# Kernel optimization log

Hardware: AMD Instinct MI355X
Metric: run time of the kernel (lower is better)

## Reference

```python
import jax, jax.numpy as jnp
import numpy as np
import math

B, S, D = 4, 2048, 1024
N_HEADS = 16
D_FF = 4096
T_DIM = 256
KEEP_RATIO = 0.7
EPS = 1e-5


def _layernorm(x):
    mu = jnp.mean(x, axis=-1, keepdims=True)
    var = jnp.mean((x - mu) ** 2, axis=-1, keepdims=True)
    return (x - mu) * jax.lax.rsqrt(var + EPS)


def _ada_ln(x, cond, W, b):
    # cond: (B, T_DIM); W: (2D, T_DIM)
    p = jax.nn.silu(cond) @ W.T + b            # (B, 2D)
    gamma, beta = jnp.split(p, 2, axis=-1)
    return _layernorm(x) * (1.0 + gamma[:, None, :]) + beta[:, None, :]


def _mha(h, in_w, in_b, out_w, out_b):
    b, s, d = h.shape
    hd = d // N_HEADS
    qkv = h @ in_w.T + in_b                     # (b, s, 3d)
    q, k, v = jnp.split(qkv, 3, axis=-1)
    def heads(t):
        return t.reshape(b, s, N_HEADS, hd).transpose(0, 2, 1, 3)
    q, k, v = heads(q), heads(k), heads(v)
    scores = jnp.einsum('bhqd,bhkd->bhqk', q, k) / math.sqrt(hd)
    attn = jax.nn.softmax(scores, axis=-1)
    o = jnp.einsum('bhqk,bhkd->bhqd', attn, v)  # (b, h, s, hd)
    o = o.transpose(0, 2, 1, 3).reshape(b, s, d)
    return o @ out_w.T + out_b


def setup_inputs() -> dict:
    key = jax.random.key(0)
    ks = jax.random.split(key, 24)
    sc = 0.02
    return {
        'x': jax.random.normal(ks[0], (B, S, D), jnp.float32),
        't_emb': jax.random.normal(ks[1], (B, T_DIM), jnp.float32),
        'tr_w1': jax.random.normal(ks[2], (32, D), jnp.float32) * sc,
        'tr_b1': jnp.zeros((32,), jnp.float32),
        'tr_w2': jax.random.normal(ks[3], (1, 32), jnp.float32) * sc,
        'tr_b2': jnp.zeros((1,), jnp.float32),
        'ln1_w': jax.random.normal(ks[4], (2 * D, T_DIM), jnp.float32) * sc,
        'ln1_b': jnp.zeros((2 * D,), jnp.float32),
        'ln2_w': jax.random.normal(ks[5], (2 * D, T_DIM), jnp.float32) * sc,
        'ln2_b': jnp.zeros((2 * D,), jnp.float32),
        'in_proj_w': jax.random.normal(ks[6], (3 * D, D), jnp.float32) * sc,
        'in_proj_b': jnp.zeros((3 * D,), jnp.float32),
        'out_w': jax.random.normal(ks[7], (D, D), jnp.float32) * sc,
        'out_b': jnp.zeros((D,), jnp.float32),
        'ffn_w1': jax.random.normal(ks[8], (D_FF, D), jnp.float32) * sc,
        'ffn_b1': jnp.zeros((D_FF,), jnp.float32),
        'ffn_w2': jax.random.normal(ks[9], (D, D_FF), jnp.float32) * sc,
        'ffn_b2': jnp.zeros((D,), jnp.float32),
        # torch inits gates to zero; use small randn so the block is non-trivial
        'gate_attn': jax.random.normal(ks[10], (1, 1, D), jnp.float32) * sc,
        'gate_ffn': jax.random.normal(ks[11], (1, 1, D), jnp.float32) * sc,
    }


def reference(x, t_emb, tr_w1, tr_b1, tr_w2, tr_b2, ln1_w, ln1_b, ln2_w, ln2_b,
              in_proj_w, in_proj_b, out_w, out_b, ffn_w1, ffn_b1, ffn_w2, ffn_b2,
              gate_attn, gate_ffn):
    b, s, d = x.shape
    num_keep = max(int(s * KEEP_RATIO), 1)

    # token importance on detached x (stop_gradient mirrors x.detach())
    xd = jax.lax.stop_gradient(x)
    imp = jax.nn.silu(xd @ tr_w1.T + tr_b1) @ tr_w2.T + tr_b2  # (b, s, 1)
    imp = imp[..., 0]
    _, idx = jax.lax.top_k(imp, num_keep)
    idx = jnp.sort(idx, axis=-1)                               # (b, num_keep)

    x_sel = jnp.take_along_axis(x, idx[..., None], axis=1)     # (b, k, d)

    h = _ada_ln(x_sel, t_emb, ln1_w, ln1_b)
    h = _mha(h, in_proj_w, in_proj_b, out_w, out_b)
    x_sel = x_sel + gate_attn * h

    h = _ada_ln(x_sel, t_emb, ln2_w, ln2_b)
    h = jax.nn.gelu(h @ ffn_w1.T + ffn_b1, approximate=False) @ ffn_w2.T + ffn_b2
    x_sel = x_sel + gate_ffn * h

    batch_idx = jnp.arange(b)[:, None]
    return x.at[batch_idx, idx].set(x_sel)
```

## Files before the change

### kernel.cpp

```cpp
#include <hip/hip_runtime.h>
#include <hip/hip_bf16.h>
#include <cmath>
#include <cstdint>

typedef __bf16 bf16;
typedef __bf16 bf16x8 __attribute__((ext_vector_type(8)));
typedef __bf16 bf16x4 __attribute__((ext_vector_type(4)));
typedef float  f32x4  __attribute__((ext_vector_type(4)));

constexpr int B_   = 4;
constexpr int S_   = 2048;
constexpr int D_   = 1024;
constexpr int H_   = 16;
constexpr int DFF_ = 4096;
constexpr int TD_  = 256;
constexpr int KEEP = 1433;
constexpr int M_TOT = B_ * KEEP;
constexpr int MPAD  = 5888;
constexpr int QT64  = (KEEP + 63) / 64;
constexpr int NKV   = (KEEP + 63) / 64;
constexpr float EPS = 1e-5f;
constexpr float QSCALE = 0.18033688011112042f;

__device__ __forceinline__ f32x4 mfma16(bf16x8 a, bf16x8 b, f32x4 c) {
  return __builtin_amdgcn_mfma_f32_16x16x32_bf16(a, b, c, 0, 0, 0);
}

#define GLOAD_LDS(gp, lp)                                                     \
  __builtin_amdgcn_global_load_lds(                                           \
      (const __attribute__((address_space(1))) void*)(gp),                    \
      (__attribute__((address_space(3))) void*)(lp), 16, 0, 0)

__global__ __launch_bounds__(256) void k_prep(
    const float* __restrict__ x, const float* __restrict__ tr_w1,
    double* __restrict__ hidden,
    const float* __restrict__ in_w, const float* __restrict__ out_w,
    const float* __restrict__ f1_w, const float* __restrict__ f2_w,
    bf16* __restrict__ w_in, bf16* __restrict__ w_out,
    bf16* __restrict__ w_f1, bf16* __restrict__ w_f2,
    float* __restrict__ dout,
    const float* __restrict__ temb,
    const float* __restrict__ ln1_w, const float* __restrict__ ln1_b,
    float* __restrict__ p1,
    const float* __restrict__ ln2_w, const float* __restrict__ ln2_b,
    float* __restrict__ p2)
{
  __shared__ double sred[4][64][17];
  const int bid = blockIdx.x;
  if (bid < 2048) {
    const int lane = threadIdx.x & 63, w = threadIdx.x >> 6;
    const int tok0 = (bid & 511) * 16 + w * 4;
    const int u0 = (bid >> 9) * 8;
    const float* xb = x + (size_t)tok0 * D_ + lane * 4;
    const float* wb = tr_w1 + (size_t)u0 * D_ + lane * 4;
    double acc[4][8] = {};
#pragma unroll 2
    for (int c = 0; c < D_; c += 256) {
      float4 xv[4], wv[8];
#pragma unroll
      for (int i = 0; i < 4; ++i)
        xv[i] = *(const float4*)(xb + (size_t)i * D_ + c);
#pragma unroll
      for (int u = 0; u < 8; ++u)
        wv[u] = *(const float4*)(wb + (size_t)u * D_ + c);
#pragma unroll
      for (int i = 0; i < 4; ++i)
#pragma unroll
        for (int u = 0; u < 8; ++u) {
          acc[i][u] += (double)xv[i].x * (double)wv[u].x;
          acc[i][u] += (double)xv[i].y * (double)wv[u].y;
          acc[i][u] += (double)xv[i].z * (double)wv[u].z;
          acc[i][u] += (double)xv[i].w * (double)wv[u].w;
        }
    }
    double* my = &sred[w][0][0];
#pragma unroll
    for (int bt = 0; bt < 2; ++bt) {
#pragma unroll
      for (int a = 0; a < 16; ++a)
        my[lane * 17 + a] = acc[2 * bt + (a >> 3)][a & 7];
      asm volatile("s_waitcnt lgkmcnt(0)" ::: "memory");
      __builtin_amdgcn_sched_barrier(0);
      const int a = lane >> 2, sl = lane & 3;
      const double* rp = my + (sl * 16) * 17 + a;
      double s0 = rp[0]        + rp[17];
      double s1 = rp[2  * 17]  + rp[3  * 17];
      double s2 = rp[4  * 17]  + rp[5  * 17];
      double s3 = rp[6  * 17]  + rp[7  * 17];
      s0 += rp[8  * 17]; s1 += rp[9  * 17];
      s2 += rp[10 * 17]; s3 += rp[11 * 17];
      s0 += rp[12 * 17]; s1 += rp[13 * 17];
      s2 += rp[14 * 17]; s3 += rp[15 * 17];
      double s = (s0 + s1) + (s2 + s3);
      s += __shfl_xor(s, 1);
      s += __shfl_xor(s, 2);
      if (sl == 0)
        hidden[(size_t)(tok0 + 2 * bt + (a >> 3)) * 32 + u0 + (a & 7)] = s;
      asm volatile("s_waitcnt lgkmcnt(0)" ::: "memory");
      __builtin_amdgcn_sched_barrier(0);
    }
  } else if (bid < 3584) {
    const int base = (bid - 2048) * 2048 + threadIdx.x;
#pragma unroll
    for (int k2 = 0; k2 < 8; ++k2) {
      const int g = base + k2 * 256;
      const float* src; bf16* dst; int off;
      if (g < 786432)       { src = in_w;  dst = w_in;  off = g; }
      else if (g < 1048576) { src = out_w; dst = w_out; off = g - 786432; }
      else if (g < 2097152) { src = f1_w;  dst = w_f1;  off = g - 1048576; }
      else                  { src = f2_w;  dst = w_f2;  off = g - 2097152; }
      float4 v = ((const float4*)src)[off];
      bf16x4 o = {(bf16)v.x, (bf16)v.y, (bf16)v.z, (bf16)v.w};
      ((bf16x4*)dst)[off] = o;
    }
  } else if (bid < 4608) {
    const int base = (bid - 3584) * 2048 + threadIdx.x;
    float4 v[8];
#pragma unroll
    for (int k2 = 0; k2 < 8; ++k2) v[k2] = ((const float4*)x)[base + k2 * 256];
#pragma unroll
    for (int k2 = 0; k2 < 8; ++k2) ((float4*)dout)[base + k2 * 256] = v[k2];
  } else {
    int gw = (int)(((bid - 4608) * 256 + threadIdx.x) >> 6);
    const int lane = threadIdx.x & 63;
    const float* W = ln1_w; const float* bias = ln1_b; float* p = p1;
    if (gw >= 8192) { gw -= 8192; W = ln2_w; bias = ln2_b; p = p2; }
    const int b = gw >> 11;
    const int row = gw & 2047;
    const float* te = temb + (size_t)b * TD_;
    const float* wr = W + (size_t)row * TD_;
    float acc = 0.f;
    for (int i = lane; i < TD_; i += 64) {
      float c = te[i];
      acc += (c / (1.f + __expf(-c))) * wr[i];
    }
    for (int o = 32; o > 0; o >>= 1) acc += __shfl_down(acc, o);
    if (lane == 0) p[(size_t)b * 2 * D_ + row] = acc + bias[row];
  }
}

__global__ __launch_bounds__(256) void k_imptail(
    const double* __restrict__ hidden, const float* __restrict__ b1,
    const float* __restrict__ w2, const float* __restrict__ b2,
    double* __restrict__ imp)
{
  const int tok = blockIdx.x * 256 + threadIdx.x;
  const double* hp = hidden + (size_t)tok * 32;
  double r = 0.0;
#pragma unroll
  for (int u = 0; u < 32; ++u) {
    double s = hp[u] + (double)b1[u];
    double sv = s / (1.0 + exp(-s));
    r += sv * (double)w2[u];
  }
  imp[tok] = r + (double)b2[0];
}

__global__ __launch_bounds__(256) void k_rank(const double* __restrict__ imp,
                                              int* __restrict__ rank)
{
  const int b = blockIdx.x >> 5;
  const int seg = blockIdx.x & 31;
  __shared__ double vals[S_];
  const double* ib = imp + (size_t)b * S_;
  for (int i = threadIdx.x; i < S_ / 2; i += 256)
    ((double2*)vals)[i] = ((const double2*)ib)[i];
  __syncthreads();
  const int tl = threadIdx.x >> 2;
  const int part = threadIdx.x & 3;
  const int s = seg * 64 + tl;
  const double v = vals[s];
  int cnt = 0;
  for (int j = part * 512; j < (part + 1) * 512; ++j) {
    double u = vals[j];
    cnt += (u > v) || (u == v && j < s);
  }
  cnt += __shfl_xor(cnt, 1);
  cnt += __shfl_xor(cnt, 2);
  if (part == 0) rank[b * S_ + s] = cnt;
}

__global__ __launch_bounds__(256) void k_compact(const int* __restrict__ rank,
                                                 int* __restrict__ idx)
{
  const int b = blockIdx.x;
  __shared__ int wcnt[4];
  __shared__ int base_s;
  if (threadIdx.x == 0) base_s = 0;
  __syncthreads();
  const int t = threadIdx.x, lane = t & 63, w = t >> 6;
  for (int c = 0; c < S_ / 256; ++c) {
    const int s = c * 256 + t;
    const bool kept = rank[b * S_ + s] < KEEP;
    unsigned long long m = __ballot(kept);
    int piw = __popcll(m & ((1ull << lane) - 1ull));
    if (lane == 0) wcnt[w] = __popcll(m);
    __syncthreads();
    int off = base_s;
    for (int i = 0; i < w; ++i) off += wcnt[i];
    if (kept) idx[b * KEEP + off + piw] = s;
    __syncthreads();
    if (t == 0) base_s += wcnt[0] + wcnt[1] + wcnt[2] + wcnt[3];
    __syncthreads();
  }
}

__global__ __launch_bounds__(256) void k_adaln(
    const float* __restrict__ xsrc, const int* __restrict__ idx,
    const float* __restrict__ p, bf16* __restrict__ hout)
{
  const int r = blockIdx.x, t = threadIdx.x;
  bf16* orow = hout + (size_t)r * D_;
  if (r >= M_TOT) {
    bf16x4 z = {(bf16)0.f, (bf16)0.f, (bf16)0.f, (bf16)0.f};
    ((bf16x4*)orow)[t] = z;
    return;
  }
  const int b = r / KEEP, j = r - b * KEEP;
  const int s = idx[b * KEEP + j];
  const float* xr = xsrc + ((size_t)(b * S_ + s)) * D_;
  float4 v = ((const float4*)xr)[t];
  __shared__ float red[8];
  float sum = v.x + v.y + v.z + v.w;
  for (int o = 32; o > 0; o >>= 1) sum += __shfl_down(sum, o);
  const int lane = t & 63, w = t >> 6;
  if (lane == 0) red[w] = sum;
  __syncthreads();
  const float mu = (red[0] + red[1] + red[2] + red[3]) * (1.f / D_);
  const float dx = v.x - mu, dy = v.y - mu, dz = v.z - mu, dw = v.w - mu;
  float vs = dx * dx + dy * dy + dz * dz + dw * dw;
  for (int o = 32; o > 0; o >>= 1) vs += __shfl_down(vs, o);
  if (lane == 0) red[4 + w] = vs;
  __syncthreads();
  const float rstd = rsqrtf((red[4] + red[5] + red[6] + red[7]) * (1.f / D_) + EPS);
  const float* gp = p + (size_t)b * 2 * D_;
  float4 g  = ((const float4*)gp)[t];
  float4 be = ((const float4*)(gp + D_))[t];
  bf16x4 o;
  o[0] = (bf16)(dx * rstd * (1.f + g.x) + be.x);
  o[1] = (bf16)(dy * rstd * (1.f + g.y) + be.y);
  o[2] = (bf16)(dz * rstd * (1.f + g.z) + be.z);
  o[3] = (bf16)(dw * rstd * (1.f + g.w) + be.w);
  ((bf16x4*)orow)[t] = o;
}

template <int BN, int MODE>
__global__ __launch_bounds__(256) void k_gemm(
    const bf16* __restrict__ A, const bf16* __restrict__ W,
    const float* __restrict__ bias, bf16* __restrict__ Cbf,
    const float* __restrict__ gate, const int* __restrict__ idx,
    float* __restrict__ resid, int N, int K, int gn)
{
  constexpr int WN = BN / 2;
  constexpr int NJ = WN / 16;
  constexpr int WIT = BN / 32;
  __shared__ bf16 As[2][128 * 64];
  __shared__ bf16 Ws[2][BN * 64];
  const int t = threadIdx.x, lane = t & 63;
  const int w = t >> 6, wr = w >> 1, wc = w & 1;
  const int fr = lane & 15, fq = lane >> 4;

  const int nwg = gridDim.x, orig = blockIdx.x;
  const int q8 = nwg >> 3, r8 = nwg & 7;
  const int xc = orig & 7, pos = orig >> 3;
  const int wgid = (xc < r8 ? xc * (q8 + 1) : r8 * (q8 + 1) + (xc - r8) * q8) + pos;
  const int bm = wgid / gn, bn = wgid - bm * gn;

  const bf16* Ab = A + (size_t)bm * 128 * K;
  const bf16* Wb = W + (size_t)bn * BN * K;

  const bf16* pA[4];
  const bf16* pW[WIT];
#pragma unroll
  for (int it = 0; it < 4; ++it) {
    const int e = it * 256 + t;
    const int row = e >> 3, pc = e & 7;
    const int lc = pc ^ (row & 7);
    pA[it] = Ab + (size_t)row * K + lc * 8;
  }
#pragma unroll
  for (int it = 0; it < WIT; ++it) {
    const int e = it * 256 + t;
    const int row = e >> 3, pc = e & 7;
    const int lc = pc ^ (row & 7);
    pW[it] = Wb + (size_t)row * K + lc * 8;
  }

  auto stage = [&](int buf) {
#pragma unroll
    for (int it = 0; it < 4; ++it) {
      GLOAD_LDS(pA[it], &As[buf][0] + (it * 256 + t) * 8);
      pA[it] += 64;
    }
#pragma unroll
    for (int it = 0; it < WIT; ++it) {
      GLOAD_LDS(pW[it], &Ws[buf][0] + (it * 256 + t) * 8);
      pW[it] += 64;
    }
  };

  f32x4 acc[4][NJ] = {};
  stage(0);
  const int nkt = K >> 6;
  int cur = 0;
  for (int kt = 0; kt < nkt; ++kt) {
    __syncthreads();
    if (kt + 1 < nkt) stage(cur ^ 1);
    const char* Al = (const char*)&As[cur][0];
    const char* Wl = (const char*)&Ws[cur][0];
#pragma unroll
    for (int kk = 0; kk < 2; ++kk) {
      bf16x8 af[4], wf[NJ];
#pragma unroll
      for (int i = 0; i < 4; ++i)
        af[i] = *(const bf16x8*)(Al + (wr * 64 + i * 16 + fr) * 128 +
                                 (((kk * 4 + fq) ^ (fr & 7)) << 4));
#pragma unroll
      for (int j = 0; j < NJ; ++j)
        wf[j] = *(const bf16x8*)(Wl + (wc * WN + j * 16 + fr) * 128 +
                                 (((kk * 4 + fq) ^ (fr & 7)) << 4));
#pragma unroll
      for (int i = 0; i < 4; ++i)
#pragma unroll
        for (int j = 0; j < NJ; ++j)
          acc[i][j] = mfma16(af[i], wf[j], acc[i][j]);
    }
    cur ^= 1;
  }

  if (MODE == 2) {
#pragma unroll
    for (int i = 0; i < 4; ++i) {
#pragma unroll
      for (int r = 0; r < 4; ++r) {
        const int m = bm * 128 + wr * 64 + i * 16 + fq * 4 + r;
        if (m < M_TOT) {
          const int b = m / KEEP, jj = m - b * KEEP;
          const int s = idx[b * KEEP + jj];
          float* rp = resid + ((size_t)(b * S_ + s)) * D_ + bn * BN + wc * WN + fr;
          const float* gp = gate + bn * BN + wc * WN + fr;
          const float* bp = bias + bn * BN + wc * WN + fr;
#pragma unroll
          for (int j = 0; j < NJ; ++j)
            rp[j * 16] += gp[j * 16] * (acc[i][j][r] + bp[j * 16]);
        }
      }
    }
  } else {
#pragma unroll
    for (int i = 0; i < 4; ++i) {
#pragma unroll
      for (int j = 0; j < NJ; ++j) {
#pragma unroll
        for (int r = 0; r < 4; ++r) {
          const int m = bm * 128 + wr * 64 + i * 16 + fq * 4 + r;
          const int n = bn * BN + wc * WN + j * 16 + fr;
          float v = acc[i][j][r] + bias[n];
          if (MODE == 0) {
            if (n < D_) v *= QSCALE;
            Cbf[(size_t)m * N + n] = (bf16)v;
          } else {
            float gl = 0.5f * v * (1.f + erff(v * 0.70710678118654752f));
            Cbf[(size_t)m * N + n] = (bf16)gl;
          }
        }
      }
    }
  }
}

__global__ __launch_bounds__(256) void k_attn(const bf16* __restrict__ qkv,
                                              bf16* __restrict__ out)
{
  __shared__ bf16 Klds[2][64 * 64];
  __shared__ bf16 Vlds[2][64 * 64];

  const int t = threadIdx.x;
  const int lane = t & 63, w = t >> 6;
  const int fr = lane & 15, fq = lane >> 4;

  const int orig = blockIdx.x;
  const int wgid = (orig & 7) * 184 + (orig >> 3);
  const int qt = wgid % QT64;
  const int hb = wgid / QT64;
  const int h = hb & 15, b = hb >> 4;

  const size_t rowbase = (size_t)b * KEEP;
  const size_t RS = 3 * D_;
  const bf16* kbase = qkv + rowbase * RS + D_ + h * 64;
  const bf16* vbase = qkv + rowbase * RS + 2 * D_ + h * 64;

  const int wq0 = qt * 64 + w * 16;
  const int qrow = min(wq0 + fr, KEEP - 1);
  const bf16* qp = qkv + (rowbase + qrow) * RS + h * 64 + fq * 8;
  const bf16x8 qf0 = *(const bf16x8*)qp;
  const bf16x8 qf1 = *(const bf16x8*)(qp + 32);

  f32x4 o[4] = {};
  float mrow = -INFINITY, lrow = 0.f;

  const int p0 = t, p1 = 256 + t;
  auto kaddr = [&](int p, int kv) {
    const int row = p >> 3, c8p = p & 7;
    const int c8 = c8p ^ ((row & 7) ^ (row >> 3));
    const int gr = min(kv + row, KEEP - 1);
    return kbase + (size_t)gr * RS + c8 * 8;
  };
  auto vaddr = [&](int p, int kv) {
    const int db = p >> 7, ksub = (p >> 3) & 15, jr = (p >> 1) & 3,
              c8lo = p & 1;
    const int vrow = ksub * 4 + jr, vc8 = db * 2 + c8lo;
    const int gr = min(kv + vrow, KEEP - 1);
    return vbase + (size_t)gr * RS + vc8 * 8;
  };
  const bf16* kp0 = kaddr(p0, 0);
  const bf16* kp1 = kaddr(p1, 0);
  const bf16* vp0 = vaddr(p0, 0);
  const bf16* vp1 = vaddr(p1, 0);

  auto stage_fast = [&](int buf) {
    GLOAD_LDS(kp0, &Klds[buf][0] + p0 * 8);
    GLOAD_LDS(kp1, &Klds[buf][0] + p1 * 8);
    GLOAD_LDS(vp0, &Vlds[buf][0] + p0 * 8);
    GLOAD_LDS(vp1, &Vlds[buf][0] + p1 * 8);
    kp0 += 64 * RS; kp1 += 64 * RS; vp0 += 64 * RS; vp1 += 64 * RS;
  };
  auto stage_last = [&](int buf, int kv) {
    GLOAD_LDS(kaddr(p0, kv), &Klds[buf][0] + p0 * 8);
    GLOAD_LDS(kaddr(p1, kv), &Klds[buf][0] + p1 * 8);
    GLOAD_LDS(vaddr(p0, kv), &Vlds[buf][0] + p0 * 8);
    GLOAD_LDS(vaddr(p1, kv), &Vlds[buf][0] + p1 * 8);
  };

  stage_fast(0);
  int cur = 0;

  const unsigned vbase_lds0 =
      (unsigned)(size_t)(__attribute__((address_space(3))) bf16*)&Vlds[0][0];
  const unsigned vbase_lds1 =
      (unsigned)(size_t)(__attribute__((address_space(3))) bf16*)&Vlds[1][0];

  for (int ti = 0; ti < NKV; ++ti) {
    const int kv = ti * 64;
    __syncthreads();
    if (ti < NKV - 2) stage_fast(cur ^ 1);
    else if (ti == NKV - 2) stage_last(cur ^ 1, kv + 64);

    const char* Kl = (const char*)&Klds[cur][0];

    f32x4 sc[4];
    __builtin_amdgcn_s_setprio(1);
#pragma unroll
    for (int f = 0; f < 4; ++f) {
      const int row = ((f >> 1) << 5) + ((fr >> 2) << 3) + ((f & 1) << 1) +
                      (fr & 1) + (((fr >> 1) & 1) << 2);
      const int swz = (row & 7) ^ (row >> 3);
      const bf16x8 kf0 = *(const bf16x8*)(Kl + row * 128 + ((fq ^ swz) << 4));
      const bf16x8 kf1 =
          *(const bf16x8*)(Kl + row * 128 + (((fq ^ 4) ^ swz) << 4));
      f32x4 s = {0.f, 0.f, 0.f, 0.f};
      s = mfma16(kf0, qf0, s);
      s = mfma16(kf1, qf1, s);
      sc[f] = s;
    }
    __builtin_amdgcn_s_setprio(0);

    const unsigned vb =
        (cur ? vbase_lds1 : vbase_lds0) + ((unsigned)fq << 7);
    bf16x4 v0[8], v1[8];
    asm volatile(
        "ds_read_b64_tr_b16 %0, %8 offset:0\n\t"
        "ds_read_b64_tr_b16 %1, %8 offset:128\n\t"
        "ds_read_b64_tr_b16 %2, %8 offset:2048\n\t"
        "ds_read_b64_tr_b16 %3, %8 offset:2176\n\t"
        "ds_read_b64_tr_b16 %4, %8 offset:4096\n\t"
        "ds_read_b64_tr_b16 %5, %8 offset:4224\n\t"
        "ds_read_b64_tr_b16 %6, %8 offset:6144\n\t"
        "ds_read_b64_tr_b16 %7, %8 offset:6272"
        : "=&v"(v0[0]), "=&v"(v0[1]), "=&v"(v0[2]), "=&v"(v0[3]),
          "=&v"(v0[4]), "=&v"(v0[5]), "=&v"(v0[6]), "=&v"(v0[7])
        : "v"(vb));
    asm volatile(
        "ds_read_b64_tr_b16 %0, %8 offset:1024\n\t"
        "ds_read_b64_tr_b16 %1, %8 offset:1152\n\t"
        "ds_read_b64_tr_b16 %2, %8 offset:3072\n\t"
        "ds_read_b64_tr_b16 %3, %8 offset:3200\n\t"
        "ds_read_b64_tr_b16 %4, %8 offset:5120\n\t"
        "ds_read_b64_tr_b16 %5, %8 offset:5248\n\t"
        "ds_read_b64_tr_b16 %6, %8 offset:7168\n\t"
        "ds_read_b64_tr_b16 %7, %8 offset:7296"
        : "=&v"(v1[0]), "=&v"(v1[1]), "=&v"(v1[2]), "=&v"(v1[3]),
          "=&v"(v1[4]), "=&v"(v1[5]), "=&v"(v1[6]), "=&v"(v1[7])
        : "v"(vb));

    if (ti == NKV - 1) {
#pragma unroll
      for (int f = 0; f < 4; ++f)
#pragma unroll
        for (int r = 0; r < 4; ++r) {
          const int kl = ((f >> 1) << 5) + (fq << 3) + ((f & 1) << 1) +
                         (r & 1) + ((r >> 1) << 2);
          if (kv + kl >= KEEP) sc[f][r] = -INFINITY;
        }
    }
    float m0 = fmaxf(fmaxf(sc[0][0], sc[0][1]), sc[0][2]);
    float m1 = fmaxf(fmaxf(sc[0][3], sc[1][0]), sc[1][1]);
    float m2 = fmaxf(fmaxf(sc[1][2], sc[1][3]), sc[2][0]);
    float m3 = fmaxf(fmaxf(sc[2][1], sc[2][2]), sc[2][3]);
    float m4 = fmaxf(fmaxf(sc[3][0], sc[3][1]), sc[3][2]);
    float mx = fmaxf(fmaxf(m0, m1), m2);
    mx = fmaxf(fmaxf(mx, m3), fmaxf(m4, sc[3][3]));
    mx = fmaxf(mx, __shfl_xor(mx, 16));
    mx = fmaxf(mx, __shfl_xor(mx, 32));

    const bool noresc = __all(mx <= mrow + 8.f);
    const float mnew = noresc ? mrow : fmaxf(mrow, mx);
    float ps = 0.f;
    bf16 pe[4][4];
#pragma unroll
    for (int f = 0; f < 4; ++f)
#pragma unroll
      for (int r = 0; r < 4; ++r) {
        const float pv = exp2f(sc[f][r] - mnew);
        ps += pv;
        pe[f][r] = (bf16)pv;
      }
    ps += __shfl_xor(ps, 16);
    ps += __shfl_xor(ps, 32);
    if (!noresc) {
      const float fac = exp2f(mrow - mnew);
      lrow *= fac;
#pragma unroll
      for (int db = 0; db < 4; ++db) {
        o[db][0] *= fac; o[db][1] *= fac; o[db][2] *= fac; o[db][3] *= fac;
      }
      mrow = mnew;
    }
    lrow += ps;

    const bf16x8 pb[2] = {
        {pe[0][0], pe[0][1], pe[1][0], pe[1][1],
         pe[0][2], pe[0][3], pe[1][2], pe[1][3]},
        {pe[2][0], pe[2][1], pe[3][0], pe[3][1],
         pe[2][2], pe[2][3], pe[3][2], pe[3][3]}};

    asm volatile("s_waitcnt lgkmcnt(0)" ::: "memory");
    __builtin_amdgcn_sched_barrier(0);

    const bf16x8 vf00 = __builtin_shufflevector(v0[0], v0[1], 0,1,2,3,4,5,6,7);
    const bf16x8 vf01 = __builtin_shufflevector(v0[2], v0[3], 0,1,2,3,4,5,6,7);
    const bf16x8 vf02 = __builtin_shufflevector(v0[4], v0[5], 0,1,2,3,4,5,6,7);
    const bf16x8 vf03 = __builtin_shufflevector(v0[6], v0[7], 0,1,2,3,4,5,6,7);
    const bf16x8 vf10 = __builtin_shufflevector(v1[0], v1[1], 0,1,2,3,4,5,6,7);
    const bf16x8 vf11 = __builtin_shufflevector(v1[2], v1[3], 0,1,2,3,4,5,6,7);
    const bf16x8 vf12 = __builtin_shufflevector(v1[4], v1[5], 0,1,2,3,4,5,6,7);
    const bf16x8 vf13 = __builtin_shufflevector(v1[6], v1[7], 0,1,2,3,4,5,6,7);
    __builtin_amdgcn_s_setprio(1);
    o[0] = mfma16(vf00, pb[0], o[0]);
    o[1] = mfma16(vf01, pb[0], o[1]);
    o[2] = mfma16(vf02, pb[0], o[2]);
    o[3] = mfma16(vf03, pb[0], o[3]);
    o[0] = mfma16(vf10, pb[1], o[0]);
    o[1] = mfma16(vf11, pb[1], o[1]);
    o[2] = mfma16(vf12, pb[1], o[2]);
    o[3] = mfma16(vf13, pb[1], o[3]);
    __builtin_amdgcn_s_setprio(0);
    cur ^= 1;
  }

  const int q = wq0 + fr;
  if (q < KEEP) {
    const float inv = 1.f / lrow;
#pragma unroll
    for (int db = 0; db < 4; ++db) {
      bf16x4 wv = {(bf16)(o[db][0] * inv), (bf16)(o[db][1] * inv),
                   (bf16)(o[db][2] * inv), (bf16)(o[db][3] * inv)};
      *(bf16x4*)(out + (rowbase + q) * (size_t)D_ + h * 64 + db * 16 + fq * 4) =
          wv;
    }
  }
}

extern "C" void kernel_launch(void* const* d_in, const int* in_sizes, int n_in,
                              void* d_out, int out_size, void* d_ws, size_t ws_size,
                              hipStream_t stream)
{
  (void)in_sizes; (void)n_in; (void)out_size; (void)ws_size;
  const float* x      = (const float*)d_in[0];
  const float* t_emb  = (const float*)d_in[1];
  const float* tr_w1  = (const float*)d_in[2];
  const float* tr_b1  = (const float*)d_in[3];
  const float* tr_w2  = (const float*)d_in[4];
  const float* tr_b2  = (const float*)d_in[5];
  const float* ln1_w  = (const float*)d_in[6];
  const float* ln1_b  = (const float*)d_in[7];
  const float* ln2_w  = (const float*)d_in[8];
  const float* ln2_b  = (const float*)d_in[9];
  const float* in_w   = (const float*)d_in[10];
  const float* in_b   = (const float*)d_in[11];
  const float* out_w  = (const float*)d_in[12];
  const float* out_b  = (const float*)d_in[13];
  const float* f1_w   = (const float*)d_in[14];
  const float* f1_b   = (const float*)d_in[15];
  const float* f2_w   = (const float*)d_in[16];
  const float* f2_b   = (const float*)d_in[17];
  const float* gate_a = (const float*)d_in[18];
  const float* gate_f = (const float*)d_in[19];

  char* ws = (char*)d_ws;
  size_t off = 0;
  auto alloc = [&](size_t bytes) -> char* {
    char* p = ws + off;
    off = (off + bytes + 255) & ~(size_t)255;
    return p;
  };
  double* imp  = (double*)alloc((size_t)B_ * S_ * 8);
  double* hid  = (double*)alloc((size_t)B_ * S_ * 32 * 8);
  int* rank    = (int*)alloc((size_t)B_ * S_ * 4);
  int* idx     = (int*)alloc((size_t)B_ * KEEP * 4);
  float* p1    = (float*)alloc((size_t)B_ * 2 * D_ * 4);
  float* p2    = (float*)alloc((size_t)B_ * 2 * D_ * 4);
  bf16* w_in   = (bf16*)alloc((size_t)3 * D_ * D_ * 2);
  bf16* w_out  = (bf16*)alloc((size_t)D_ * D_ * 2);
  bf16* w_f1   = (bf16*)alloc((size_t)DFF_ * D_ * 2);
  bf16* w_f2   = (bf16*)alloc((size_t)D_ * DFF_ * 2);
  bf16* h_bf   = (bf16*)alloc((size_t)MPAD * D_ * 2);
  bf16* big    = (bf16*)alloc((size_t)MPAD * (3 * D_ + D_) * 2);
  bf16* qkv    = big;
  bf16* attn   = big + (size_t)MPAD * 3 * D_;
  bf16* ffn1   = big;

  k_prep<<<8704, 256, 0, stream>>>(
      x, tr_w1, hid,
      in_w, out_w, f1_w, f2_w, w_in, w_out, w_f1, w_f2,
      (float*)d_out,
      t_emb, ln1_w, ln1_b, p1, ln2_w, ln2_b, p2);
  k_imptail<<<B_ * S_ / 256, 256, 0, stream>>>(hid, tr_b1, tr_w2, tr_b2, imp);
  k_rank<<<B_ * 32, 256, 0, stream>>>(imp, rank);
  k_compact<<<B_, 256, 0, stream>>>(rank, idx);

  k_adaln<<<MPAD, 256, 0, stream>>>(x, idx, p1, h_bf);
  k_gemm<128, 0><<<46 * 24, 256, 0, stream>>>(
      h_bf, w_in, in_b, qkv, nullptr, nullptr, nullptr, 3 * D_, D_, 24);
  k_attn<<<QT64 * H_ * B_, 256, 0, stream>>>(qkv, attn);
  k_gemm<64, 2><<<46 * 16, 256, 0, stream>>>(
      attn, w_out, out_b, nullptr, gate_a, idx, (float*)d_out, D_, D_, 16);
  k_adaln<<<MPAD, 256, 0, stream>>>((const float*)d_out, idx, p2, h_bf);
  k_gemm<128, 1><<<46 * 32, 256, 0, stream>>>(
      h_bf, w_f1, f1_b, ffn1, nullptr, nullptr, nullptr, DFF_, D_, 32);
  k_gemm<64, 2><<<46 * 16, 256, 0, stream>>>(
      ffn1, w_f2, f2_b, nullptr, gate_f, idx, (float*)d_out, D_, DFF_, 16);
}
```

Baseline: 407.7 us.

## Enlarge attention query tile to 128 rows with 512-thread workgroups

The attention kernel now processes 128 query rows per workgroup using 8 waves instead of 64 rows with 4 waves, so each K/V tile staged in LDS is shared by twice as many query rows. Each thread now issues one K and one V async load per tile instead of two, and the grid shrinks to half as many workgroups with an adjusted XCD swizzle (96 per XCD). This halves redundant K/V global traffic, at the cost of fewer, larger workgroups (768 total) and a larger tail in the last query tile (1433 rows padded to 1536).

```diff
diff --git a/kernel.cpp b/kernel.cpp
--- a/kernel.cpp
+++ b/kernel.cpp
@@ -17,7 +17,7 @@
 constexpr int KEEP = 1433;
 constexpr int M_TOT = B_ * KEEP;
 constexpr int MPAD  = 5888;
-constexpr int QT64  = (KEEP + 63) / 64;
+constexpr int QT128 = (KEEP + 127) / 128;
 constexpr int NKV   = (KEEP + 63) / 64;
 constexpr float EPS = 1e-5f;
 constexpr float QSCALE = 0.18033688011112042f;
@@ -369,7 +369,7 @@
   }
 }
 
-__global__ __launch_bounds__(256) void k_attn(const bf16* __restrict__ qkv,
+__global__ __launch_bounds__(512) void k_attn(const bf16* __restrict__ qkv,
                                               bf16* __restrict__ out)
 {
   __shared__ bf16 Klds[2][64 * 64];
@@ -380,9 +380,9 @@
   const int fr = lane & 15, fq = lane >> 4;
 
   const int orig = blockIdx.x;
-  const int wgid = (orig & 7) * 184 + (orig >> 3);
-  const int qt = wgid % QT64;
-  const int hb = wgid / QT64;
+  const int wgid = (orig & 7) * 96 + (orig >> 3);
+  const int qtb = wgid % QT128;
+  const int hb = wgid / QT128;
   const int h = hb & 15, b = hb >> 4;
 
   const size_t rowbase = (size_t)b * KEEP;
@@ -390,7 +390,7 @@
   const bf16* kbase = qkv + rowbase * RS + D_ + h * 64;
   const bf16* vbase = qkv + rowbase * RS + 2 * D_ + h * 64;
 
-  const int wq0 = qt * 64 + w * 16;
+  const int wq0 = qtb * 128 + w * 16;
   const int qrow = min(wq0 + fr, KEEP - 1);
   const bf16* qp = qkv + (rowbase + qrow) * RS + h * 64 + fq * 8;
   const bf16x8 qf0 = *(const bf16x8*)qp;
@@ -399,7 +399,6 @@
   f32x4 o[4] = {};
   float mrow = -INFINITY, lrow = 0.f;
 
-  const int p0 = t, p1 = 256 + t;
   auto kaddr = [&](int p, int kv) {
     const int row = p >> 3, c8p = p & 7;
     const int c8 = c8p ^ ((row & 7) ^ (row >> 3));
@@ -413,23 +412,17 @@
     const int gr = min(kv + vrow, KEEP - 1);
     return vbase + (size_t)gr * RS + vc8 * 8;
   };
-  const bf16* kp0 = kaddr(p0, 0);
-  const bf16* kp1 = kaddr(p1, 0);
-  const bf16* vp0 = vaddr(p0, 0);
-  const bf16* vp1 = vaddr(p1, 0);
+  const bf16* kp = kaddr(t, 0);
+  const bf16* vp = vaddr(t, 0);
 
   auto stage_fast = [&](int buf) {
-    GLOAD_LDS(kp0, &Klds[buf][0] + p0 * 8);
-    GLOAD_LDS(kp1, &Klds[buf][0] + p1 * 8);
-    GLOAD_LDS(vp0, &Vlds[buf][0] + p0 * 8);
-    GLOAD_LDS(vp1, &Vlds[buf][0] + p1 * 8);
-    kp0 += 64 * RS; kp1 += 64 * RS; vp0 += 64 * RS; vp1 += 64 * RS;
+    GLOAD_LDS(kp, &Klds[buf][0] + t * 8);
+    GLOAD_LDS(vp, &Vlds[buf][0] + t * 8);
+    kp += 64 * RS; vp += 64 * RS;
   };
   auto stage_last = [&](int buf, int kv) {
-    GLOAD_LDS(kaddr(p0, kv), &Klds[buf][0] + p0 * 8);
-    GLOAD_LDS(kaddr(p1, kv), &Klds[buf][0] + p1 * 8);
-    GLOAD_LDS(vaddr(p0, kv), &Vlds[buf][0] + p0 * 8);
-    GLOAD_LDS(vaddr(p1, kv), &Vlds[buf][0] + p1 * 8);
+    GLOAD_LDS(kaddr(t, kv), &Klds[buf][0] + t * 8);
+    GLOAD_LDS(vaddr(t, kv), &Vlds[buf][0] + t * 8);
   };
 
   stage_fast(0);
@@ -642,7 +635,7 @@
   k_adaln<<<MPAD, 256, 0, stream>>>(x, idx, p1, h_bf);
   k_gemm<128, 0><<<46 * 24, 256, 0, stream>>>(
       h_bf, w_in, in_b, qkv, nullptr, nullptr, nullptr, 3 * D_, D_, 24);
-  k_attn<<<QT64 * H_ * B_, 256, 0, stream>>>(qkv, attn);
+  k_attn<<<QT128 * H_ * B_, 512, 0, stream>>>(qkv, attn);
   k_gemm<64, 2><<<46 * 16, 256, 0, stream>>>(
       attn, w_out, out_b, nullptr, gate_a, idx, (float*)d_out, D_, D_, 16);
   k_adaln<<<MPAD, 256, 0, stream>>>((const float*)d_out, idx, p2, h_bf);
```

New measurement: 402.5 us. No clear change (-1.3%).
